# Kernel tuning notes

Hardware: AMD Instinct MI355X
Metric: run time of the kernel (lower is better)

## Reference

```python
import jax, jax.numpy as jnp
import numpy as np

FILTER_LENGTH = 8192
COND_DIM = 16
BATCH = 32
SEQ_LEN = 262144


def setup_inputs() -> dict:
    key = jax.random.key(0)
    k1, k2, k3, k4, k5, k6 = jax.random.split(key, 6)
    inputs = jax.random.normal(k1, (BATCH, SEQ_LEN, 1), dtype=jnp.float32)
    c = jax.random.normal(k2, (BATCH, 1, COND_DIM), dtype=jnp.float32)
    # learned linear layers: filters (magnitude net) and phase net
    Wf = jax.random.normal(k3, (FILTER_LENGTH, COND_DIM), dtype=jnp.float32) * 0.02
    bf = jax.random.normal(k4, (FILTER_LENGTH,), dtype=jnp.float32) * 0.02
    Wp = jax.random.normal(k5, (FILTER_LENGTH, COND_DIM), dtype=jnp.float32) * 0.02
    bp = jax.random.normal(k6, (FILTER_LENGTH,), dtype=jnp.float32) * 0.02
    return {"inputs": inputs, "c": c, "Wf": Wf, "bf": bf, "Wp": Wp, "bp": bp}


def reference(inputs, c, Wf, bf, Wp, bp):
    B, S, _ = inputs.shape
    FL = Wf.shape[0]
    bs = FL // 2  # block_size = filter_length // 2 (hop size of overlap-add)

    cvec = c[:, 0, :]  # (B, cond_dim)
    mag = jax.nn.sigmoid(cvec @ Wf.T + bf)   # (B, FL)
    phase = cvec @ Wp.T + bp                 # (B, FL)
    H = mag * jnp.exp(1j * phase)            # complex64 frequency response, (B, FL)

    # left-pad input by FL-1 zeros, as in the torch module
    xp = jnp.pad(inputs[:, :, 0], ((0, 0), (FL - 1, 0)))  # (B, S + FL - 1)

    nb = S // bs  # seq_len is a multiple of block_size
    blocks = xp[:, :nb * bs].reshape(B, nb, bs)           # non-overlapping input blocks

    X = jnp.fft.fft(blocks, n=FL, axis=-1)                # zero-pad each block to FL
    Yb = jnp.fft.ifft(X * H[:, None, :], axis=-1)         # (B, nb, FL) complex

    # overlap-add: block k covers output [k*bs, k*bs + FL); FL == 2*bs, so the
    # first halves tile [0, nb*bs) and the second halves tile [bs, nb*bs + bs).
    y = jnp.zeros((B, nb * bs + bs), dtype=Yb.dtype)
    y = y.at[:, : nb * bs].add(Yb[:, :, :bs].reshape(B, nb * bs))
    y = y.at[:, bs:].add(Yb[:, :, bs:].reshape(B, nb * bs))

    return jnp.real(y[:, :S])[:, :, None]  # (B, S, 1)
```

## Files before the change

kernel.cpp:

```cpp
#include <hip/hip_runtime.h>
#include <hip/hip_fp16.h>
#include <math.h>

#define FL     8192
#define BS     4096
#define CD     16
#define BATCH  32
#define SEQ    262144
#define NPAIR  32
#define LDSN   8448

typedef float vf2 __attribute__((ext_vector_type(2)));
__device__ __forceinline__ vf2 mkv(float x, float y){ vf2 v; v.x = x; v.y = y; return v; }
__device__ __forceinline__ vf2 cmul(vf2 a, vf2 b){
    const vf2 c = mkv(-a.y, a.x) * mkv(b.y, b.y);
    return a * mkv(b.x, b.x) + c;
}
__device__ __forceinline__ vf2 mri(vf2 a, float c, float s){
    const vf2 t = mkv(-a.y, a.x) * mkv(s, s);
    return a * mkv(c, c) + t;
}

__device__ __forceinline__ void sth(__half2* buf, int i, vf2 v){ buf[i] = __floats2half2_rn(v.x, v.y); }
__device__ __forceinline__ vf2 ldh(const __half2* buf, int i){ const float2 f = __half22float2(buf[i]); return mkv(f.x, f.y); }

__device__ __forceinline__ int pos_of_bin(int k){
    return ((k&15)<<9) | (((k>>4)&15)<<5) | (k>>8);
}

template<bool INV, bool HALF, int S>
__device__ __forceinline__ void dft16(vf2* d){
    constexpr float sgn = INV ? 1.f : -1.f;
    constexpr float C1 = 0.923879532511287f;
    constexpr float S1 = 0.382683432365090f;
    constexpr float R  = 0.707106781186548f;
    vf2 u[16];
#pragma unroll
    for (int b=0;b<4;++b){
        const vf2 a0=d[S*b], a1=d[S*(4+b)];
        if (HALF){
            const vf2 ja1 = mkv(-sgn*a1.y, sgn*a1.x);
            u[4*b+0]=a0+a1;
            u[4*b+1]=a0+ja1;
            u[4*b+2]=a0-a1;
            u[4*b+3]=a0-ja1;
        } else {
            const vf2 a2=d[S*(8+b)], a3=d[S*(12+b)];
            const vf2 s0=a0+a2, s1=a0-a2;
            const vf2 s2=a1+a3, s3=a1-a3;
            const vf2 js3 = mkv(-sgn*s3.y, sgn*s3.x);
            u[4*b+0]=s0+s2;
            u[4*b+1]=s1+js3;
            u[4*b+2]=s0-s2;
            u[4*b+3]=s1-js3;
        }
    }
    u[4+1] = mri(u[4+1],  C1, sgn*S1);
    u[4+2] = mri(u[4+2],  R,  sgn*R );
    u[4+3] = mri(u[4+3],  S1, sgn*C1);
    u[8+1] = mri(u[8+1],  R,  sgn*R );
    u[8+2] = mri(u[8+2],  0.f, sgn);
    u[8+3] = mri(u[8+3], -R,  sgn*R );
    u[12+1]= mri(u[12+1], S1, sgn*C1);
    u[12+2]= mri(u[12+2],-R,  sgn*R );
    u[12+3]= mri(u[12+3],-C1,-sgn*S1);
#pragma unroll
    for (int c=0;c<4;++c){
        const vf2 a0=u[c], a1=u[4+c], a2=u[8+c], a3=u[12+c];
        const vf2 s0=a0+a2, s1=a0-a2;
        const vf2 s2=a1+a3, s3=a1-a3;
        const vf2 js3 = mkv(-sgn*s3.y, sgn*s3.x);
        d[S*(c+0)] =s0+s2;
        d[S*(c+4)] =s1+js3;
        d[S*(c+8)] =s0-s2;
        d[S*(c+12)]=s1-js3;
    }
}

__device__ __forceinline__ void tw_apply(vf2* d, vf2 w1){
    vf2 w[16];
    w[1] = w1;
#pragma unroll
    for (int q=2;q<16;++q) w[q] = cmul(w[q>>1], w[q-(q>>1)]);
#pragma unroll
    for (int q=1;q<16;++q) d[q] = cmul(d[q], w[q]);
}
__device__ __forceinline__ void tw_apply2(vf2* d, vf2 w1){
    vf2 w[16];
    w[1] = w1;
#pragma unroll
    for (int q=2;q<16;++q) w[q] = cmul(w[q>>1], w[q-(q>>1)]);
#pragma unroll
    for (int q=1;q<16;++q){ d[q] = cmul(d[q], w[q]); d[16+q] = cmul(d[16+q], w[q]); }
}

__global__ void h_kernel(const float* __restrict__ c,  const float* __restrict__ Wf,
                         const float* __restrict__ bfv, const float* __restrict__ Wp,
                         const float* __restrict__ bpv, float2* __restrict__ H,
                         float4* __restrict__ outz){
    const int f = blockIdx.x*256 + threadIdx.x;
    const int b = blockIdx.y;
    const int g = (FL - f) & (FL - 1);

    {
        const int gtid = (blockIdx.y*gridDim.x + blockIdx.x)*256 + threadIdx.x;
        const float4 z = make_float4(0.f,0.f,0.f,0.f);
#pragma unroll
        for (int i=0;i<16;++i) outz[gtid + i*131072] = z;
    }

    float amf = bfv[f], apf = bpv[f], amg = bfv[g], apg = bpv[g];
#pragma unroll
    for (int i=0;i<CD;++i){
        const float cv = c[b*CD + i];
        amf += cv * Wf[f*CD + i];
        apf += cv * Wp[f*CD + i];
        amg += cv * Wf[g*CD + i];
        apg += cv * Wp[g*CD + i];
    }
    const float magf = 1.f/(1.f+__expf(-amf));
    const float magg = 1.f/(1.f+__expf(-amg));
    float sf, cf2, sg, cg2;
    __sincosf(apf, &sf, &cf2);
    __sincosf(apg, &sg, &cg2);
    const float scale = 0.5f / (float)FL;
    const float re = (magf*cf2 + magg*cg2)*scale;
    const float im = (magf*sf  - magg*sg )*scale;
    float2* Hb = H + (size_t)b*FL;
    Hb[pos_of_bin(f)] = make_float2(re,  im);
    Hb[pos_of_bin(g)] = make_float2(re, -im);
    if (f == 0){
        float am = bfv[4096], ap = bpv[4096];
#pragma unroll
        for (int i=0;i<CD;++i){
            const float cv = c[b*CD + i];
            am += cv * Wf[4096*CD + i];
            ap += cv * Wp[4096*CD + i];
        }
        const float mag = 1.f/(1.f+__expf(-am));
        Hb[pos_of_bin(4096)] = make_float2(mag*__cosf(ap)*(2.f*scale), 0.f);
    }
}

__global__ __launch_bounds__(256, 3) void fft_kernel(const float*  __restrict__ x,
                                                     const float2* __restrict__ H,
                                                     float* __restrict__ out){
    extern __shared__ __half2 buf[];
    const int t  = threadIdx.x;
    const int pr = blockIdx.x;
    const int b  = blockIdx.y;
    const float* xb = x + (size_t)b*SEQ;
    const int s0 = 2*pr*BS - (FL-1);
    const float TWO_PI = 6.28318530717958647692f;

    vf2 d[32];

    constexpr float CT[16] = { 1.f, 0.980785280403230f, 0.923879532511287f, 0.831469612302545f,
                               0.707106781186548f, 0.555570233019602f, 0.382683432365090f, 0.195090322016128f,
                               0.f,-0.195090322016128f,-0.382683432365090f,-0.555570233019602f,
                              -0.707106781186548f,-0.831469612302545f,-0.923879532511287f,-0.980785280403230f };
    constexpr float ST[16] = { 0.f, 0.195090322016128f, 0.382683432365090f, 0.555570233019602f,
                               0.707106781186548f, 0.831469612302545f, 0.923879532511287f, 0.980785280403230f,
                               1.f, 0.980785280403230f, 0.923879532511287f, 0.831469612302545f,
                               0.707106781186548f, 0.555570233019602f, 0.382683432365090f, 0.195090322016128f };

    const int pa0 = t + (t>>5);

    {
        if (pr == 0){
#pragma unroll
            for (int h=0; h<2; ++h){
                const int j = t + 256*h;
#pragma unroll
                for (int m=0;m<8;++m){
                    const int k  = j + 512*m;
                    const int ua = s0 + k, ub = ua + BS;
                    const float va = (ua >= 0) ? xb[ua] : 0.f;
                    const float vb = (ub >= 0) ? xb[ub] : 0.f;
                    d[16*h + m] = mkv(va, vb);
                }
            }
        } else {
            const float* bp = xb + s0;
#pragma unroll
            for (int h=0; h<2; ++h){
                const int j = t + 256*h;
#pragma unroll
                for (int m=0;m<8;++m){
                    const int k = j + 512*m;
                    d[16*h + m] = mkv(bp[k], bp[k + BS]);
                }
            }
        }
        dft16<false,true,1>(d);
        dft16<false,true,1>(d+16);
        float sn, cs; __sincosf(-TWO_PI * (float)t / 8192.f, &sn, &cs);
        const vf2 w0 = mkv(cs, sn);
        tw_apply(d,    w0);
        tw_apply(d+16, cmul(w0, mkv(0.980785280403230f, -0.195090322016128f)));
#pragma unroll
        for (int q=0;q<16;++q){
            sth(buf, pa0       + 528*q, d[q]);
            sth(buf, pa0 + 264 + 528*q, d[16+q]);
        }
    }
    __syncthreads();

    {
        const int j2 = t & 31;
        const int a0 = 528*(t>>5) + j2;
        const int a1 = a0 + 4224;
#pragma unroll
        for (int m=0;m<16;++m){
            d[m]    = ldh(buf, a0 + 33*m);
            d[16+m] = ldh(buf, a1 + 33*m);
        }
        dft16<false,false,1>(d);
        dft16<false,false,1>(d+16);
        float sn, cs; __sincosf(-TWO_PI * (float)j2 / 512.f, &sn, &cs);
        tw_apply2(d, mkv(cs, sn));
#pragma unroll
        for (int q=0;q<16;++q){
            sth(buf, a0 + 33*q, d[q]);
            sth(buf, a1 + 33*q, d[16+q]);
        }
    }
    __syncthreads();

    {
        const int a0 = 33*t;
#pragma unroll
        for (int i=0;i<32;++i) d[i] = ldh(buf, a0 + i);
        dft16<false,false,2>(d);
        dft16<false,false,2>(d+1);
        const float2* Hb = H + (size_t)b*FL + (t<<5);
#pragma unroll
        for (int w=0;w<16;++w){
            const vf2 Ow = mri(d[2*w+1], CT[w], -ST[w]);
            const vf2 Ew = d[2*w];
            vf2 Xlo = Ew + Ow;
            vf2 Xhi = Ew - Ow;
            const float2 h0 = Hb[w], h1 = Hb[w+16];
            Xlo = cmul(Xlo, mkv(h0.x, h0.y));
            Xhi = cmul(Xhi, mkv(h1.x, h1.y));
            d[2*w]   = Xlo + Xhi;
            d[2*w+1] = mri(Xlo - Xhi, CT[w], ST[w]);
        }
        dft16<true,false,2>(d);
        dft16<true,false,2>(d+1);
#pragma unroll
        for (int i=0;i<32;++i) sth(buf, a0 + i, d[i]);
    }
    __syncthreads();

    {
        const int j2 = t & 31;
        const int a0 = 528*(t>>5) + j2;
        const int a1 = a0 + 4224;
#pragma unroll
        for (int q=0;q<16;++q){
            d[q]    = ldh(buf, a0 + 33*q);
            d[16+q] = ldh(buf, a1 + 33*q);
        }
        float sn, cs; __sincosf(TWO_PI * (float)j2 / 512.f, &sn, &cs);
        tw_apply2(d, mkv(cs, sn));
        dft16<true,false,1>(d);
        dft16<true,false,1>(d+16);
#pragma unroll
        for (int m=0;m<16;++m){
            sth(buf, a0 + 33*m, d[m]);
            sth(buf, a1 + 33*m, d[16+m]);
        }
    }
    __syncthreads();

    {
#pragma unroll
        for (int q=0;q<16;++q){
            d[q]    = ldh(buf, pa0       + 528*q);
            d[16+q] = ldh(buf, pa0 + 264 + 528*q);
        }
        float sn, cs; __sincosf(TWO_PI * (float)t / 8192.f, &sn, &cs);
        const vf2 w0 = mkv(cs, sn);
        tw_apply(d,    w0);
        tw_apply(d+16, cmul(w0, mkv(0.980785280403230f, 0.195090322016128f)));
        dft16<true,false,1>(d);
        dft16<true,false,1>(d+16);
        float* ob = out + (size_t)b*SEQ;
        const int pa = 2*pr*BS;
        const bool last = (pr == NPAIR-1);
#pragma unroll
        for (int h=0; h<2; ++h){
            const int j = t + 256*h;
#pragma unroll
            for (int mm=0;mm<8;++mm){
                const int klo = j + 512*mm;
                const vf2 ylo = d[16*h + mm];
                const vf2 yhi = d[16*h + mm + 8];
                atomicAdd(&ob[pa+klo], ylo.x);
                ob[pa+BS+klo] = yhi.x + ylo.y;
                if (!last) atomicAdd(&ob[pa+2*BS+klo], yhi.y);
            }
        }
    }
}

extern "C" void kernel_launch(void* const* d_in, const int* in_sizes, int n_in,
                              void* d_out, int out_size, void* d_ws, size_t ws_size,
                              hipStream_t stream) {
    const float* x   = (const float*)d_in[0];
    const float* c   = (const float*)d_in[1];
    const float* Wf  = (const float*)d_in[2];
    const float* bfv = (const float*)d_in[3];
    const float* Wp  = (const float*)d_in[4];
    const float* bpv = (const float*)d_in[5];

    float*  out = (float*)d_out;
    float2* H   = (float2*)d_ws;

    h_kernel<<<dim3(FL/2/256, BATCH), 256, 0, stream>>>(c, Wf, bfv, Wp, bpv, H,
                                                        (float4*)d_out);
    fft_kernel<<<dim3(NPAIR, BATCH), 256, LDSN*sizeof(__half2), stream>>>(x, H, out);
}
```

Before: 57.61 us.

## Pad LDS rows to stride 36 for vectorized 128-bit half2 access, trim zero-fill

Changes the LDS row stride from 33 to 36 half2 elements so each thread's 32-element row is 16-byte aligned. The middle FFT stage can then read and write its row with eight uint4 accesses instead of 32 scalar ones. The zero-fill in h_kernel now clears only half the output region, through a remapped index, presumably because the other half is written fully by the main kernel. The stride change adds some LDS footprint and may bring back bank conflicts that the old 33 padding avoided.

```diff
diff --git a/kernel.cpp b/kernel.cpp
--- a/kernel.cpp
+++ b/kernel.cpp
@@ -8,7 +8,8 @@
 #define BATCH  32
 #define SEQ    262144
 #define NPAIR  32
-#define LDSN   8448
+#define BSTR   36
+#define LDSN   (256*BSTR)
 
 typedef float vf2 __attribute__((ext_vector_type(2)));
 __device__ __forceinline__ vf2 mkv(float x, float y){ vf2 v; v.x = x; v.y = y; return v; }
@@ -23,6 +24,8 @@
 
 __device__ __forceinline__ void sth(__half2* buf, int i, vf2 v){ buf[i] = __floats2half2_rn(v.x, v.y); }
 __device__ __forceinline__ vf2 ldh(const __half2* buf, int i){ const float2 f = __half22float2(buf[i]); return mkv(f.x, f.y); }
+__device__ __forceinline__ vf2 h2f(unsigned u){ const float2 f = __half22float2(__builtin_bit_cast(__half2, u)); return mkv(f.x, f.y); }
+__device__ __forceinline__ unsigned f2h(vf2 v){ return __builtin_bit_cast(unsigned, __floats2half2_rn(v.x, v.y)); }
 
 __device__ __forceinline__ int pos_of_bin(int k){
     return ((k&15)<<9) | (((k>>4)&15)<<5) | (k>>8);
@@ -106,7 +109,11 @@
         const int gtid = (blockIdx.y*gridDim.x + blockIdx.x)*256 + threadIdx.x;
         const float4 z = make_float4(0.f,0.f,0.f,0.f);
 #pragma unroll
-        for (int i=0;i<16;++i) outz[gtid + i*131072] = z;
+        for (int k=0;k<8;++k){
+            const int i  = gtid + k*131072;
+            const int ei = ((i>>10)<<11) | (i&1023);
+            outz[ei] = z;
+        }
     }
 
     float amf = bfv[f], apf = bpv[f], amg = bfv[g], apg = bpv[g];
@@ -164,7 +171,7 @@
                                1.f, 0.980785280403230f, 0.923879532511287f, 0.831469612302545f,
                                0.707106781186548f, 0.555570233019602f, 0.382683432365090f, 0.195090322016128f };
 
-    const int pa0 = t + (t>>5);
+    const int pa0 = BSTR*(t>>5) + (t&31);
 
     {
         if (pr == 0){
@@ -200,20 +207,20 @@
         tw_apply(d+16, cmul(w0, mkv(0.980785280403230f, -0.195090322016128f)));
 #pragma unroll
         for (int q=0;q<16;++q){
-            sth(buf, pa0       + 528*q, d[q]);
-            sth(buf, pa0 + 264 + 528*q, d[16+q]);
+            sth(buf, pa0       + 576*q, d[q]);
+            sth(buf, pa0 + 288 + 576*q, d[16+q]);
         }
     }
     __syncthreads();
 
     {
         const int j2 = t & 31;
-        const int a0 = 528*(t>>5) + j2;
-        const int a1 = a0 + 4224;
+        const int a0 = 576*(t>>5) + j2;
+        const int a1 = a0 + 4608;
 #pragma unroll
         for (int m=0;m<16;++m){
-            d[m]    = ldh(buf, a0 + 33*m);
-            d[16+m] = ldh(buf, a1 + 33*m);
+            d[m]    = ldh(buf, a0 + BSTR*m);
+            d[16+m] = ldh(buf, a1 + BSTR*m);
         }
         dft16<false,false,1>(d);
         dft16<false,false,1>(d+16);
@@ -221,16 +228,20 @@
         tw_apply2(d, mkv(cs, sn));
 #pragma unroll
         for (int q=0;q<16;++q){
-            sth(buf, a0 + 33*q, d[q]);
-            sth(buf, a1 + 33*q, d[16+q]);
+            sth(buf, a0 + BSTR*q, d[q]);
+            sth(buf, a1 + BSTR*q, d[16+q]);
         }
     }
     __syncthreads();
 
     {
-        const int a0 = 33*t;
-#pragma unroll
-        for (int i=0;i<32;++i) d[i] = ldh(buf, a0 + i);
+        const uint4* __restrict__ srcv = reinterpret_cast<const uint4*>(buf + BSTR*t);
+#pragma unroll
+        for (int k=0;k<8;++k){
+            const uint4 v = srcv[k];
+            d[4*k+0] = h2f(v.x); d[4*k+1] = h2f(v.y);
+            d[4*k+2] = h2f(v.z); d[4*k+3] = h2f(v.w);
+        }
         dft16<false,false,2>(d);
         dft16<false,false,2>(d+1);
         const float2* Hb = H + (size_t)b*FL + (t<<5);
@@ -248,19 +259,25 @@
         }
         dft16<true,false,2>(d);
         dft16<true,false,2>(d+1);
-#pragma unroll
-        for (int i=0;i<32;++i) sth(buf, a0 + i, d[i]);
+        uint4* __restrict__ dstv = reinterpret_cast<uint4*>(buf + BSTR*t);
+#pragma unroll
+        for (int k=0;k<8;++k){
+            uint4 v;
+            v.x = f2h(d[4*k+0]); v.y = f2h(d[4*k+1]);
+            v.z = f2h(d[4*k+2]); v.w = f2h(d[4*k+3]);
+            dstv[k] = v;
+        }
     }
     __syncthreads();
 
     {
         const int j2 = t & 31;
-        const int a0 = 528*(t>>5) + j2;
-        const int a1 = a0 + 4224;
+        const int a0 = 576*(t>>5) + j2;
+        const int a1 = a0 + 4608;
 #pragma unroll
         for (int q=0;q<16;++q){
-            d[q]    = ldh(buf, a0 + 33*q);
-            d[16+q] = ldh(buf, a1 + 33*q);
+            d[q]    = ldh(buf, a0 + BSTR*q);
+            d[16+q] = ldh(buf, a1 + BSTR*q);
         }
         float sn, cs; __sincosf(TWO_PI * (float)j2 / 512.f, &sn, &cs);
         tw_apply2(d, mkv(cs, sn));
@@ -268,8 +285,8 @@
         dft16<true,false,1>(d+16);
 #pragma unroll
         for (int m=0;m<16;++m){
-            sth(buf, a0 + 33*m, d[m]);
-            sth(buf, a1 + 33*m, d[16+m]);
+            sth(buf, a0 + BSTR*m, d[m]);
+            sth(buf, a1 + BSTR*m, d[16+m]);
         }
     }
     __syncthreads();
@@ -277,8 +294,8 @@
     {
 #pragma unroll
         for (int q=0;q<16;++q){
-            d[q]    = ldh(buf, pa0       + 528*q);
-            d[16+q] = ldh(buf, pa0 + 264 + 528*q);
+            d[q]    = ldh(buf, pa0       + 576*q);
+            d[16+q] = ldh(buf, pa0 + 288 + 576*q);
         }
         float sn, cs; __sincosf(TWO_PI * (float)t / 8192.f, &sn, &cs);
         const vf2 w0 = mkv(cs, sn);
```

Result: no change. 56.81 us, median of 2 (-1.4%).
